# Kernel tuning notes

Measured on AMD Instinct MI355X. Metric: run time of the kernel, lower is better.

The kernel has to match this reference:

```python
import jax, jax.numpy as jnp
import numpy as np

N_E = 16384
E_DIM = 64
GROUPS = 4
N_E_GROUP = N_E // GROUPS  # 4096
B, H, W = 16, 32, 32


def _l2norm(x):
    # matches F.normalize(p=2, dim=-1) with eps=1e-12
    n = jnp.linalg.norm(x, axis=-1, keepdims=True)
    return x / jnp.maximum(n, 1e-12)


def setup_inputs() -> dict:
    key = jax.random.key(0)
    k1, k2 = jax.random.split(key)
    z_groups = jax.random.normal(k1, (B, GROUPS * E_DIM, H, W), dtype=jnp.float32)
    emb = jax.random.uniform(k2, (N_E, E_DIM), minval=-1.0 / N_E, maxval=1.0 / N_E,
                             dtype=jnp.float32)
    emb = _l2norm(emb)  # module normalizes codebook at init when l2_norm=True
    return {"z_groups": z_groups, "embedding": emb}


def reference(z_groups, embedding):
    # Eval-mode forward (no EMA/random-restart buffer updates, losses are 0).
    b, c, h, w = z_groups.shape
    # split channels into groups: b (g*c) h w -> b h w g c
    z = z_groups.reshape(b, GROUPS, E_DIM, h, w).transpose(0, 3, 4, 1, 2)
    z = _l2norm(z)                                     # l2_norm=True path
    zf = z.reshape(-1, GROUPS, E_DIM)                  # [N, g, c]
    emb = _l2norm(embedding.reshape(GROUPS, N_E_GROUP, E_DIM))  # [g, k, c]

    # d = -|z|^2 - |e|^2 + 2 z.e  (negative squared distance), argmax = nearest
    d = (2.0 * jnp.einsum('ngc,gkc->ngk', zf, emb)
         - jnp.sum(zf * zf, axis=-1)[..., None]
         - jnp.sum(emb * emb, axis=-1)[None, :, :])    # [N, g, k]
    idx = jnp.argmax(d, axis=-1)                       # [N, g]

    zq = emb[jnp.arange(GROUPS)[None, :], idx]         # [N, g, c] gather
    zq = zf + jax.lax.stop_gradient(zq - zf)           # straight-through

    # b h w g c -> b (g*c) h w
    quant = zq.reshape(b, h, w, GROUPS, E_DIM).transpose(0, 3, 4, 1, 2)
    quant = quant.reshape(b, GROUPS * E_DIM, h, w)

    vq_loss = jnp.zeros((GROUPS,), jnp.float32)
    commit_loss = jnp.zeros((GROUPS,), jnp.float32)
    codebook_usage = jnp.zeros((GROUPS,), jnp.float32)

    # perplexity / min_encodings correspond to the last group (loop semantics)
    min_encodings = jax.nn.one_hot(idx[:, -1], N_E_GROUP, dtype=quant.dtype)
    avg_probs = jnp.mean(min_encodings, axis=0)
    perplexity = jnp.exp(-jnp.sum(avg_probs * jnp.log(avg_probs + 1e-10)))

    return (quant, vq_loss, commit_loss, codebook_usage,
            perplexity, min_encodings, idx)
```

## Files before the change

kernel.cpp:

```cpp
#include <hip/hip_runtime.h>
#include <hip/hip_bf16.h>
#include <math.h>

#define N_E      16384
#define E_DIM    64
#define GROUPS   4
#define N_E_G    4096
#define NQ       16384

#define OFF_QUANT   0L
#define OFF_VQLOSS  4194304L
#define OFF_PERP    4194316L
#define OFF_MINENC  4194317L
#define OFF_IDX     71303181L

#define WS_EN     0L
#define WS_EN2    1048576L
#define WS_ENHI   1064960L
#define WS_HIST   1589248L
#define WS_IDX3   1593344L

typedef float  float4v  __attribute__((ext_vector_type(4)));
typedef short  short8   __attribute__((ext_vector_type(8)));

static __device__ __forceinline__ ushort f2bf(float x) {
    union { __hip_bfloat16 h; ushort u; } cv; cv.h = __float2bfloat16(x);
    return cv.u;
}

__global__ void norm_emb_kernel(const float* __restrict__ emb,
                                float* __restrict__ en, float* __restrict__ en2,
                                ushort* __restrict__ ehi, int* __restrict__ hist) {
    const int t = threadIdx.x;
    if (blockIdx.x == 4096) {
        for (int i = t; i < N_E_G; i += 256) hist[i] = 0;
        return;
    }
    int gid  = blockIdx.x * 256 + t;
    int code = gid >> 6;
    int k    = t & 63;
    float x = emb[code * 64 + k];
    float ss = x * x;
    #pragma unroll
    for (int off = 32; off; off >>= 1) ss += __shfl_xor(ss, off, 64);
    float v = x / fmaxf(sqrtf(ss), 1e-12f);
    en[code * 64 + k]  = v;
    ehi[code * 64 + k] = f2bf(v);
    float s2 = v * v;
    #pragma unroll
    for (int off = 32; off; off >>= 1) s2 += __shfl_xor(s2, off, 64);
    if (k == 0) en2[code] = s2;
}

#define CAP  64
#define TAU  0.017f
__global__ __launch_bounds__(512, 4)
void vq_cand_kernel(const float* __restrict__ z, const ushort* __restrict__ ehi,
                    const float* __restrict__ en, const float* __restrict__ en2,
                    float* __restrict__ out,
                    int* __restrict__ hist, int* __restrict__ idx3) {
    __shared__ float  ztile[64][129];
    __shared__ float  rden[128];
    __shared__ int    cnt[128];
    __shared__ ushort cand[128 * CAP];
    __shared__ int    bks[128];

    const int g  = blockIdx.y;
    const int q0 = blockIdx.x * 128;
    const int t  = threadIdx.x;
    const int wave = t >> 6, lane = t & 63;
    const int l15 = lane & 15, quad = lane >> 4;
    const int qh = wave & 3;
    const int cq = wave >> 2;

    const int sliceId = g * 128 + blockIdx.x;
    float4v* fill4 = (float4v*)(out + OFF_VQLOSS) + (size_t)sliceId * 32768;
    const float4v z4 = {0.f, 0.f, 0.f, 0.f};

    {
        int b = q0 >> 10, hw0 = q0 & 1023;
        const float* zsrc = z + (size_t)b * 262144 + (size_t)g * 65536 + hw0;
        for (int i = t; i < 64 * 128; i += 512) {
            int d = i >> 7, q = i & 127;
            ztile[d][q] = zsrc[(size_t)d * 1024 + q];
        }
    }
    if (t < 128) cnt[t] = 0;
    __syncthreads();

    if (t < 128) {
        float ss = 0.f;
        for (int d = 0; d < 64; ++d) {
            float x = ztile[d][t];
            ss = fmaf(x, x, ss);
        }
        rden[t] = fmaxf(sqrtf(ss), 1e-12f);
    }
    __syncthreads();

    short8 bfrag[2][2];
    #pragma unroll
    for (int u = 0; u < 2; ++u) {
        int q = qh * 32 + u * 16 + l15;
        float den = rden[q];
        #pragma unroll
        for (int ks = 0; ks < 2; ++ks) {
            short8 f;
            #pragma unroll
            for (int j = 0; j < 8; ++j) {
                int k = ks * 32 + quad * 8 + j;
                f[j] = (short)f2bf(ztile[k][q] / den);
            }
            bfrag[u][ks] = f;
        }
    }

    const ushort* abase = ehi + (size_t)g * N_E_G * 64
                        + (size_t)(cq * 64 + l15) * 64 + quad * 8;

    float Mrun[2];
    Mrun[0] = -3.4e38f; Mrun[1] = -3.4e38f;

    for (int tile = 0; tile < 32; ++tile) {
        short8 af[4][2];
        {
            const ushort* p = abase + (size_t)(tile * 128) * 64;
            #pragma unroll
            for (int cs = 0; cs < 4; ++cs)
                #pragma unroll
                for (int ks = 0; ks < 2; ++ks)
                    af[cs][ks] = *(const short8*)(p + (size_t)(cs * 16) * 64 + ks * 32);
        }
        fill4[(size_t)(tile * 2 + 0) * 512 + t] = z4;
        fill4[(size_t)(tile * 2 + 1) * 512 + t] = z4;

        float4v acc[4][2];
        #pragma unroll
        for (int cs = 0; cs < 4; ++cs)
            #pragma unroll
            for (int u = 0; u < 2; ++u) {
                float4v zz = {0.f, 0.f, 0.f, 0.f};
                float4v tmp = __builtin_amdgcn_mfma_f32_16x16x32_bf16(
                                  af[cs][0], bfrag[u][0], zz, 0, 0, 0);
                acc[cs][u] = __builtin_amdgcn_mfma_f32_16x16x32_bf16(
                                  af[cs][1], bfrag[u][1], tmp, 0, 0, 0);
            }

        const int j0 = tile * 128;
        #pragma unroll
        for (int u = 0; u < 2; ++u) {
            float m = acc[0][u][0];
            #pragma unroll
            for (int cs = 0; cs < 4; ++cs)
                #pragma unroll
                for (int r = 0; r < 4; ++r) m = fmaxf(m, acc[cs][u][r]);
            float m2 = fmaxf(m, __shfl_xor(m, 16, 64));
            float m4 = fmaxf(m2, __shfl_xor(m2, 32, 64));
            Mrun[u] = fmaxf(Mrun[u], m4);
            float thr = Mrun[u] - TAU;
            if (m >= thr) {
                int ql = qh * 32 + u * 16 + l15;
                #pragma unroll
                for (int cs = 0; cs < 4; ++cs)
                    #pragma unroll
                    for (int r = 0; r < 4; ++r)
                        if (acc[cs][u][r] >= thr) {
                            int cidx = j0 + cq * 64 + cs * 16 + quad * 4 + r;
                            int slot = atomicAdd(&cnt[ql], 1);
                            if (slot < CAP) cand[ql * CAP + slot] = (ushort)cidx;
                        }
            }
        }
    }

    if (sliceId == 0 && t < 13) out[OFF_VQLOSS + 67108864L + t] = 0.f;
    __syncthreads();

    if (t < 128) {
        int q = q0 + t;
        float den = rden[t];
        float za[64];
        #pragma unroll
        for (int k = 0; k < 64; ++k) za[k] = ztile[k][t] / den;
        int nc = cnt[t]; if (nc > CAP) nc = CAP;
        float best = -3.4e38f; int bk = 0x7fffffff;
        for (int s = 0; s < nc; ++s) {
            int c = cand[t * CAP + s];
            const float* ev = en + ((size_t)g * N_E_G + c) * 64;
            float a = 0.f;
            #pragma unroll
            for (int k = 0; k < 64; ++k) a = fmaf(za[k], ev[k], a);
            float d = 2.f * a - en2[g * N_E_G + c];
            if (d > best || (d == best && c < bk)) { best = d; bk = c; }
        }
        if (bk == 0x7fffffff) bk = 0;
        bks[t] = bk;
        out[OFF_IDX + (size_t)q * 4 + g] = (float)bk;
        if (g == 3) {
            idx3[q] = bk;
            atomicAdd(&hist[bk], 1);
        }
    }
    __syncthreads();

    for (int i = t; i < 128 * 64; i += 512) {
        int d = i >> 7, m = i & 127;
        int n = q0 + m, b = n >> 10, hw = n & 1023;
        out[OFF_QUANT + (size_t)b * 262144 + (size_t)(g * 64 + d) * 1024 + hw] =
            en[((size_t)g * N_E_G + bks[m]) * 64 + d];
    }
}

__global__ void finalize_kernel(const int* __restrict__ idx3,
                                const int* __restrict__ hist,
                                float* __restrict__ out) {
    if (blockIdx.x < 64) {
        int r = blockIdx.x * 256 + threadIdx.x;
        out[OFF_MINENC + (size_t)r * N_E_G + idx3[r]] = 1.0f;
        return;
    }
    __shared__ float s[256];
    int t = threadIdx.x;
    float acc = 0.f;
    for (int k = t; k < N_E_G; k += 256) {
        float p = (float)hist[k] * (1.0f / 16384.0f);
        acc += p * logf(p + 1e-10f);
    }
    s[t] = acc;
    __syncthreads();
    for (int o = 128; o; o >>= 1) {
        if (t < o) s[t] += s[t + o];
        __syncthreads();
    }
    if (t == 0) out[OFF_PERP] = expf(-s[0]);
}

extern "C" void kernel_launch(void* const* d_in, const int* in_sizes, int n_in,
                              void* d_out, int out_size, void* d_ws, size_t ws_size,
                              hipStream_t stream) {
    const float* z_groups = (const float*)d_in[0];
    const float* emb      = (const float*)d_in[1];
    float* out = (float*)d_out;
    float* ws  = (float*)d_ws;

    float*  en   = ws + WS_EN;
    float*  en2  = ws + WS_EN2;
    ushort* ehi  = (ushort*)(ws + WS_ENHI);
    int*    hist = (int*)(ws + WS_HIST);
    int*    idx3 = (int*)(ws + WS_IDX3);

    norm_emb_kernel<<<4097, 256, 0, stream>>>(emb, en, en2, ehi, hist);

    vq_cand_kernel<<<dim3(NQ / 128, GROUPS), 512, 0, stream>>>(
        z_groups, ehi, en, en2, out, hist, idx3);

    finalize_kernel<<<65, 256, 0, stream>>>(idx3, hist, out);
}
```

Measured before the change: 436.0 us.

## Pre-swizzle bf16 codebook into MFMA fragment order and split fp32 rescoring across threads

The normalize kernel now writes the bf16 codebook in the exact per-lane MFMA fragment order, so each wave's A-fragment load becomes a contiguous coalesced read. The wave split changes from 4 query-halves by 2 code-quarters to 2 by 4, with each wave holding 4 query fragments, which gives more reuse of the loaded codes. Each wave also tracks its bf16 argmax per query and appends it as a guaranteed candidate, and CAP grows from 64 to 96. The fp32 rescoring now uses all 512 threads, four per query, followed by a shared-memory reduction. This spreads out the previously 128-thread serial tail, at the cost of extra registers and LDS.

```diff
diff --git a/kernel.cpp b/kernel.cpp
--- a/kernel.cpp
+++ b/kernel.cpp
@@ -27,6 +27,7 @@
     union { __hip_bfloat16 h; ushort u; } cv; cv.h = __float2bfloat16(x);
     return cv.u;
 }
+
 
 __global__ void norm_emb_kernel(const float* __restrict__ emb,
                                 float* __restrict__ en, float* __restrict__ en2,
@@ -44,16 +45,24 @@
     #pragma unroll
     for (int off = 32; off; off >>= 1) ss += __shfl_xor(ss, off, 64);
     float v = x / fmaxf(sqrtf(ss), 1e-12f);
-    en[code * 64 + k]  = v;
-    ehi[code * 64 + k] = f2bf(v);
+    en[code * 64 + k] = v;
+    {
+        int g = code >> 12, c = code & 4095;
+        int tile = c >> 7, cq = (c >> 5) & 3, cs = (c >> 4) & 1, l15 = c & 15;
+        int ks = k >> 5, quad = (k >> 3) & 3, j = k & 7;
+        int lane2 = quad * 16 + l15;
+        size_t off = ((size_t)(((tile * 4 + cq) * 2 + cs) * 2 + ks) * 64 + lane2) * 8 + j;
+        ehi[(size_t)g * 262144 + off] = f2bf(v);
+    }
     float s2 = v * v;
     #pragma unroll
     for (int off = 32; off; off >>= 1) s2 += __shfl_xor(s2, off, 64);
     if (k == 0) en2[code] = s2;
 }
 
-#define CAP  64
-#define TAU  0.017f
+#define CAP   96
+#define CAPT  100
+#define TAU   0.017f
 __global__ __launch_bounds__(512, 4)
 void vq_cand_kernel(const float* __restrict__ z, const ushort* __restrict__ ehi,
                     const float* __restrict__ en, const float* __restrict__ en2,
@@ -62,16 +71,19 @@
     __shared__ float  ztile[64][129];
     __shared__ float  rden[128];
     __shared__ int    cnt[128];
-    __shared__ ushort cand[128 * CAP];
+    __shared__ ushort cand[128 * CAPT];
     __shared__ int    bks[128];
+    __shared__ float  pv[512];
+    __shared__ int    pk[512];
 
     const int g  = blockIdx.y;
     const int q0 = blockIdx.x * 128;
     const int t  = threadIdx.x;
-    const int wave = t >> 6, lane = t & 63;
+    const int lane = t & 63;
+    const int wave = t >> 6;
     const int l15 = lane & 15, quad = lane >> 4;
-    const int qh = wave & 3;
-    const int cq = wave >> 2;
+    const int qh = wave & 1;
+    const int cq = wave >> 1;
 
     const int sliceId = g * 128 + blockIdx.x;
     float4v* fill4 = (float4v*)(out + OFF_VQLOSS) + (size_t)sliceId * 32768;
@@ -98,10 +110,10 @@
     }
     __syncthreads();
 
-    short8 bfrag[2][2];
-    #pragma unroll
-    for (int u = 0; u < 2; ++u) {
-        int q = qh * 32 + u * 16 + l15;
+    short8 bfrag[4][2];
+    #pragma unroll
+    for (int u = 0; u < 4; ++u) {
+        int q = qh * 64 + u * 16 + l15;
         float den = rden[q];
         #pragma unroll
         for (int ks = 0; ks < 2; ++ks) {
@@ -115,30 +127,31 @@
         }
     }
 
-    const ushort* abase = ehi + (size_t)g * N_E_G * 64
-                        + (size_t)(cq * 64 + l15) * 64 + quad * 8;
-
-    float Mrun[2];
-    Mrun[0] = -3.4e38f; Mrun[1] = -3.4e38f;
+    const ushort* gbase = ehi + (size_t)g * 262144;
+
+    float Mrun[4];
+    float pbv[4];
+    int   pbk[4];
+    #pragma unroll
+    for (int u = 0; u < 4; ++u) { Mrun[u] = -3.4e38f; pbv[u] = -3.4e38f; pbk[u] = 0; }
 
     for (int tile = 0; tile < 32; ++tile) {
-        short8 af[4][2];
-        {
-            const ushort* p = abase + (size_t)(tile * 128) * 64;
-            #pragma unroll
-            for (int cs = 0; cs < 4; ++cs)
-                #pragma unroll
-                for (int ks = 0; ks < 2; ++ks)
-                    af[cs][ks] = *(const short8*)(p + (size_t)(cs * 16) * 64 + ks * 32);
-        }
+        short8 af[2][2];
+        #pragma unroll
+        for (int cs = 0; cs < 2; ++cs)
+            #pragma unroll
+            for (int ks = 0; ks < 2; ++ks) {
+                size_t o = ((size_t)(((tile * 4 + cq) * 2 + cs) * 2 + ks) * 64 + lane) * 8;
+                af[cs][ks] = *(const short8*)(gbase + o);
+            }
         fill4[(size_t)(tile * 2 + 0) * 512 + t] = z4;
         fill4[(size_t)(tile * 2 + 1) * 512 + t] = z4;
 
-        float4v acc[4][2];
-        #pragma unroll
-        for (int cs = 0; cs < 4; ++cs)
-            #pragma unroll
-            for (int u = 0; u < 2; ++u) {
+        float4v acc[2][4];
+        #pragma unroll
+        for (int cs = 0; cs < 2; ++cs)
+            #pragma unroll
+            for (int u = 0; u < 4; ++u) {
                 float4v zz = {0.f, 0.f, 0.f, 0.f};
                 float4v tmp = __builtin_amdgcn_mfma_f32_16x16x32_bf16(
                                   af[cs][0], bfrag[u][0], zz, 0, 0, 0);
@@ -146,46 +159,65 @@
                                   af[cs][1], bfrag[u][1], tmp, 0, 0, 0);
             }
 
-        const int j0 = tile * 128;
-        #pragma unroll
-        for (int u = 0; u < 2; ++u) {
+        const int j0 = tile * 128 + cq * 32;
+        #pragma unroll
+        for (int u = 0; u < 4; ++u) {
             float m = acc[0][u][0];
             #pragma unroll
-            for (int cs = 0; cs < 4; ++cs)
+            for (int cs = 0; cs < 2; ++cs)
                 #pragma unroll
-                for (int r = 0; r < 4; ++r) m = fmaxf(m, acc[cs][u][r]);
+                for (int r = 0; r < 4; ++r) {
+                    float v = acc[cs][u][r];
+                    m = fmaxf(m, v);
+                    int ci = j0 + cs * 16 + quad * 4 + r;
+                    if (v > pbv[u] || (v == pbv[u] && ci < pbk[u])) {
+                        pbv[u] = v; pbk[u] = ci;
+                    }
+                }
             float m2 = fmaxf(m, __shfl_xor(m, 16, 64));
             float m4 = fmaxf(m2, __shfl_xor(m2, 32, 64));
             Mrun[u] = fmaxf(Mrun[u], m4);
             float thr = Mrun[u] - TAU;
             if (m >= thr) {
-                int ql = qh * 32 + u * 16 + l15;
+                int ql = qh * 64 + u * 16 + l15;
                 #pragma unroll
-                for (int cs = 0; cs < 4; ++cs)
+                for (int cs = 0; cs < 2; ++cs)
                     #pragma unroll
                     for (int r = 0; r < 4; ++r)
                         if (acc[cs][u][r] >= thr) {
-                            int cidx = j0 + cq * 64 + cs * 16 + quad * 4 + r;
+                            int cidx = j0 + cs * 16 + quad * 4 + r;
                             int slot = atomicAdd(&cnt[ql], 1);
-                            if (slot < CAP) cand[ql * CAP + slot] = (ushort)cidx;
+                            if (slot < CAP) cand[ql * CAPT + slot] = (ushort)cidx;
                         }
             }
         }
     }
 
-    if (sliceId == 0 && t < 13) out[OFF_VQLOSS + 67108864L + t] = 0.f;
-    __syncthreads();
-
-    if (t < 128) {
-        int q = q0 + t;
-        float den = rden[t];
+    #pragma unroll
+    for (int u = 0; u < 4; ++u) {
+        #pragma unroll
+        for (int off = 16; off <= 32; off <<= 1) {
+            float ov = __shfl_xor(pbv[u], off, 64);
+            int   ok = __shfl_xor(pbk[u], off, 64);
+            if (ov > pbv[u] || (ov == pbv[u] && ok < pbk[u])) { pbv[u] = ov; pbk[u] = ok; }
+        }
+        if (quad == 0) {
+            int ql = qh * 64 + u * 16 + l15;
+            cand[ql * CAPT + CAP + cq] = (ushort)pbk[u];
+        }
+    }
+    __syncthreads();
+
+    {
+        int tr = t >> 7, q = t & 127;
+        float den = rden[q];
         float za[64];
         #pragma unroll
-        for (int k = 0; k < 64; ++k) za[k] = ztile[k][t] / den;
-        int nc = cnt[t]; if (nc > CAP) nc = CAP;
+        for (int k = 0; k < 64; ++k) za[k] = ztile[k][q] / den;
+        int nc = cnt[q]; if (nc > CAP) nc = CAP;
         float best = -3.4e38f; int bk = 0x7fffffff;
-        for (int s = 0; s < nc; ++s) {
-            int c = cand[t * CAP + s];
+        for (int s = tr; s < nc + 4; s += 4) {
+            int c = (s < nc) ? cand[q * CAPT + s] : cand[q * CAPT + CAP + (s - nc)];
             const float* ev = en + ((size_t)g * N_E_G + c) * 64;
             float a = 0.f;
             #pragma unroll
@@ -193,8 +225,19 @@
             float d = 2.f * a - en2[g * N_E_G + c];
             if (d > best || (d == best && c < bk)) { best = d; bk = c; }
         }
-        if (bk == 0x7fffffff) bk = 0;
+        pv[t] = best; pk[t] = bk;
+    }
+    __syncthreads();
+
+    if (t < 128) {
+        float best = pv[t]; int bk = pk[t];
+        #pragma unroll
+        for (int tr = 1; tr < 4; ++tr) {
+            float v = pv[tr * 128 + t]; int c = pk[tr * 128 + t];
+            if (v > best || (v == best && c < bk)) { best = v; bk = c; }
+        }
         bks[t] = bk;
+        int q = q0 + t;
         out[OFF_IDX + (size_t)q * 4 + g] = (float)bk;
         if (g == 3) {
             idx3[q] = bk;
@@ -209,6 +252,8 @@
         out[OFF_QUANT + (size_t)b * 262144 + (size_t)(g * 64 + d) * 1024 + hw] =
             en[((size_t)g * N_E_G + bks[m]) * 64 + d];
     }
+
+    if (sliceId == 0 && t < 13) out[OFF_VQLOSS + 67108864L + t] = 0.f;
 }
 
 __global__ void finalize_kernel(const int* __restrict__ idx3,
```

After: 422.6 us. -3.1%, faster.
